# Performance work log

Hardware: AMD Instinct MI355X
Metric: run time of the kernel (lower is better)

## Reference

```python
import jax, jax.numpy as jnp
import numpy as np

B, S, H, NH = 2, 2048, 1024, 16
HD = H // NH  # 64


def setup_inputs() -> dict:
    key = jax.random.key(0)
    ks = jax.random.split(key, 12)
    sc = 0.02
    return {
        "query": jax.random.normal(ks[0], (B, S, H), dtype=jnp.float32),
        "key": jax.random.normal(ks[1], (B, S, H), dtype=jnp.float32),
        "value": jax.random.normal(ks[2], (B, S, H), dtype=jnp.float32),
        "attention_mask": jnp.zeros((B, S, S), dtype=jnp.float32),
        "Wq": jax.random.normal(ks[3], (H, H), dtype=jnp.float32) * sc,
        "bq": jnp.zeros((H,), dtype=jnp.float32),
        "Wk": jax.random.normal(ks[4], (H, H), dtype=jnp.float32) * sc,
        "bk": jnp.zeros((H,), dtype=jnp.float32),
        "Wv": jax.random.normal(ks[5], (H, H), dtype=jnp.float32) * sc,
        "bv": jnp.zeros((H,), dtype=jnp.float32),
        "Wo": jax.random.normal(ks[6], (H, H), dtype=jnp.float32) * sc,
        "bo": jnp.zeros((H,), dtype=jnp.float32),
    }


def reference(query, key, value, attention_mask, Wq, bq, Wk, bk, Wv, bv, Wo, bo):
    b = query.shape[0]
    # linear projections
    q = query @ Wq + bq
    k = key @ Wk + bk
    v = value @ Wv + bv
    # [b, s, h] -> [b, nh, s, hd]
    def split_heads(x):
        return x.reshape(b, -1, NH, HD).transpose(0, 2, 1, 3)
    q, k, v = split_heads(q), split_heads(k), split_heads(v)
    # scaled dot-product attention with materialized score matrix (faithful)
    scores = jnp.einsum("bhqd,bhkd->bhqk", q, k) / jnp.sqrt(jnp.float32(HD))
    scores = scores + attention_mask[:, None, :, :]
    weights = jax.nn.softmax(scores, axis=-1)  # dropout p=0 (eval)
    out = jnp.einsum("bhqk,bhkd->bhqd", weights, v)
    out = out.transpose(0, 2, 1, 3).reshape(b, -1, H)
    return out @ Wo + bo
```

## Files before the change

### kernel.cpp

```cpp
#include <hip/hip_runtime.h>
#include <hip/hip_bf16.h>
#include <math.h>

#define S_  2048
#define H_  1024
#define NH_ 16
#define HD_ 64
#define MM  4096
#define NB_ 2
#define NT_ (S_ / 64)
#define LOG2E 1.44269504088896340736f
#define SMFIX 32.0f

typedef __attribute__((ext_vector_type(8))) short bf16x8;
typedef __attribute__((ext_vector_type(4))) float f32x4;
typedef __attribute__((ext_vector_type(16))) float f32x16;
typedef __attribute__((ext_vector_type(4))) unsigned short us4;
typedef __attribute__((ext_vector_type(8))) unsigned short us8;
typedef __attribute__((ext_vector_type(2))) unsigned uint2v;

__device__ __forceinline__ void gld_lds16(const void* g, void* l) {
    __builtin_amdgcn_global_load_lds(
        (const __attribute__((address_space(1))) unsigned int*)g,
        (__attribute__((address_space(3))) unsigned int*)l, 16, 0, 0);
}

__device__ __forceinline__ unsigned short f2bf(float f) {
    union { float f; unsigned int u; } v; v.f = f;
    unsigned int r = v.u + 0x7FFFu + ((v.u >> 16) & 1u);
    return (unsigned short)(r >> 16);
}

__device__ __forceinline__ unsigned pkbf(float lo, float hi) {
    __hip_bfloat162 h = __float22bfloat162_rn(make_float2(lo, hi));
    unsigned u; __builtin_memcpy(&u, &h, 4); return u;
}

__device__ __forceinline__ float exp2_fast(float x) {
    float r; asm("v_exp_f32 %0, %1" : "=v"(r) : "v"(x)); return r;
}

__global__ __launch_bounds__(256)
void prep_kernel(const float* __restrict__ query, const float* __restrict__ key,
                 const float* __restrict__ value,
                 unsigned short* __restrict__ Xq, unsigned short* __restrict__ Xk,
                 unsigned short* __restrict__ Xv,
                 const float* __restrict__ W0, const float* __restrict__ W1,
                 const float* __restrict__ W2, const float* __restrict__ W3,
                 unsigned short* __restrict__ T0, unsigned short* __restrict__ T1,
                 unsigned short* __restrict__ T2, unsigned short* __restrict__ T3)
{
    __shared__ float t[32][33];
    const int id = blockIdx.x, tid = threadIdx.x;

    if (id < 6144) {
        const int z = id >> 11;
        const float* s = z == 0 ? query : z == 1 ? key : value;
        unsigned short* d = z == 0 ? Xq : z == 1 ? Xk : Xv;
        const int i = (id & 2047) * 256 + tid;
        float4 a = ((const float4*)s)[(size_t)i * 2];
        float4 b = ((const float4*)s)[(size_t)i * 2 + 1];
        union { unsigned u[4]; us8 v; } o;
        o.u[0] = pkbf(a.x, a.y); o.u[1] = pkbf(a.z, a.w);
        o.u[2] = pkbf(b.x, b.y); o.u[3] = pkbf(b.z, b.w);
        ((us8*)d)[i] = o.v;
    } else {
        const int rid = id - 6144;
        const int z = rid >> 10, rem = rid & 1023;
        const int n0 = (rem & 31) * 32, k0 = (rem >> 5) * 32;
        const float* W = z == 0 ? W0 : z == 1 ? W1 : z == 2 ? W2 : W3;
        unsigned short* T = z == 0 ? T0 : z == 1 ? T1 : z == 2 ? T2 : T3;
        const int tx = tid & 31, ty = tid >> 5;
        #pragma unroll
        for (int u = 0; u < 4; u++)
            t[ty + u * 8][tx] = W[(size_t)(k0 + ty + u * 8) * H_ + n0 + tx];
        __syncthreads();
        #pragma unroll
        for (int u = 0; u < 4; u++)
            T[(size_t)(n0 + ty + u * 8) * H_ + k0 + tx] = f2bf(t[tx][ty + u * 8]);
    }
}

__device__ __forceinline__
void gemm_body(unsigned short* As, unsigned short* Bs, int n0, int m0,
               const unsigned short* __restrict__ A, const unsigned short* __restrict__ Bt,
               const float* __restrict__ bias, void* __restrict__ out, float scale, int epi)
{
    const int tid = threadIdx.x;
    const int lane = tid & 63, w = tid >> 6;
    const int lane16 = lane & 15, lg = lane >> 4;
    const int wm = w & 1, wn = w >> 1;

    f32x4 acc[4][4];
    #pragma unroll
    for (int m = 0; m < 4; m++)
        #pragma unroll
        for (int n = 0; n < 4; n++) acc[m][n] = (f32x4){0.f, 0.f, 0.f, 0.f};

    auto stage = [&](int kt) {
        #pragma unroll
        for (int u = 0; u < 4; u++) {
            const int seg = w * 4 + u;
            const int L = seg * 1024 + lane * 16;
            const int row = L >> 7;
            const int blk = (L >> 4) & 7;
            const int goff = kt * 64 + ((blk ^ (row & 7)) << 3);
            gld_lds16(A  + (size_t)(m0 + row) * 1024 + goff, (char*)As + L);
            gld_lds16(Bt + (size_t)(n0 + row) * 1024 + goff, (char*)Bs + L);
        }
    };

    stage(0);
    for (int kt = 0; kt < 16; kt++) {
        __syncthreads();
        #pragma unroll
        for (int ks = 0; ks < 2; ks++) {
            const int kb = ks * 64 + lg * 16;
            bf16x8 a[4], b[4];
            #pragma unroll
            for (int m = 0; m < 4; m++) {
                const int row = wm * 64 + m * 16 + lane16;
                a[m] = *(const bf16x8*)((const char*)As + row * 128 + (kb ^ ((row & 7) << 4)));
            }
            #pragma unroll
            for (int n = 0; n < 4; n++) {
                const int row = wn * 64 + n * 16 + lane16;
                b[n] = *(const bf16x8*)((const char*)Bs + row * 128 + (kb ^ ((row & 7) << 4)));
            }
            #pragma unroll
            for (int m = 0; m < 4; m++)
                #pragma unroll
                for (int n = 0; n < 4; n++)
                    acc[m][n] = __builtin_amdgcn_mfma_f32_16x16x32_bf16(a[m], b[n], acc[m][n], 0, 0, 0);
        }
        __syncthreads();
        if (kt + 1 < 16) stage(kt + 1);
    }

    #pragma unroll
    for (int n = 0; n < 4; n++) {
        const int col = n0 + wn * 64 + n * 16 + lane16;
        const float bs = bias[col];
        #pragma unroll
        for (int m = 0; m < 4; m++) {
            const int rowb = m0 + wm * 64 + m * 16 + lg * 4;
            if (epi == 0) {
                const int nh = col >> 6, hd = col & 63;
                #pragma unroll
                for (int j = 0; j < 4; j++) {
                    const int row = rowb + j;
                    const int bb = row >> 11, s = row & 2047;
                    ((unsigned short*)out)[((((size_t)bb * NH_ + nh) * S_ + s) << 6) + hd] =
                        f2bf((acc[m][n][j] + bs) * scale);
                }
            } else if (epi == 1) {
                const int nh = col >> 6, hd = col & 63;
                const int bb = rowb >> 11, s = rowb & 2047;
                us4 o;
                #pragma unroll
                for (int j = 0; j < 4; j++) o[j] = f2bf(acc[m][n][j] + bs);
                *(us4*)&((unsigned short*)out)[((((size_t)bb * NH_ + nh) * HD_ + hd) << 11) + s] = o;
            } else {
                #pragma unroll
                for (int j = 0; j < 4; j++)
                    ((float*)out)[(size_t)(rowb + j) * H_ + col] = acc[m][n][j] + bs;
            }
        }
    }
}

__global__ __launch_bounds__(256)
void gemm_qkv_mtr(const unsigned short* __restrict__ Xq, const unsigned short* __restrict__ Xk,
                  const unsigned short* __restrict__ Xv,
                  const unsigned short* __restrict__ Wtq, const unsigned short* __restrict__ Wtk,
                  const unsigned short* __restrict__ Wtv,
                  const float* __restrict__ bq, const float* __restrict__ bk,
                  const float* __restrict__ bv,
                  unsigned short* __restrict__ qh, unsigned short* __restrict__ kh,
                  unsigned short* __restrict__ vt, float qscale,
                  const float* __restrict__ M, unsigned short* __restrict__ MT2)
{
    __shared__ __align__(16) unsigned short As[128 * 64];
    __shared__ __align__(16) unsigned short Bs[128 * 64];

    const int id = blockIdx.x, tid = threadIdx.x;

    if (id < 768) {
        const int z = id >> 8, rem = id & 255;
        const int n0 = (rem & 7) * 128, m0 = (rem >> 3) * 128;
        const unsigned short* A  = z == 0 ? Xq : z == 1 ? Xk : Xv;
        const unsigned short* Bt = z == 0 ? Wtq : z == 1 ? Wtk : Wtv;
        const float* bias        = z == 0 ? bq : z == 1 ? bk : bv;
        void* out                = z == 0 ? (void*)qh : z == 1 ? (void*)kh : (void*)vt;
        gemm_body(As, Bs, n0, m0, A, Bt, bias, out, z == 0 ? qscale : 1.0f,
                  z == 2 ? 1 : 0);
    } else {
        float (*t)[33] = (float(*)[33])As;
        const int rid = id - 768;
        const int bz = rid >> 11, rem = rid & 2047;
        const int q0 = (rem & 31) * 64, t2 = rem >> 5;
        const int kv0 = (t2 >> 1) * 64 + (t2 & 1) * 32;
        const float* Mb = M + (size_t)bz * S_ * S_;
        #pragma unroll
        for (int u = 0; u < 2; u++) {
            const int f4 = tid + u * 256;
            const int r = f4 >> 3, c = (f4 & 7) * 4;
            float4 v = *(const float4*)(Mb + (size_t)(q0 + r) * S_ + kv0 + c);
            t[r][c + 0] = v.x; t[r][c + 1] = v.y; t[r][c + 2] = v.z; t[r][c + 3] = v.w;
        }
        __syncthreads();
        const int lg2 = tid >> 7, rem2 = tid & 127;
        const int q = rem2 >> 1, half = rem2 & 1;
        union { unsigned u[4]; us8 v; } o;
        #pragma unroll
        for (int w = 0; w < 4; w++) {
            const int i0 = half * 8 + 2 * w;
            const int kc0 = (i0 & 3) + 8 * (i0 >> 2) + 4 * lg2;
            const int i1 = i0 + 1;
            const int kc1 = (i1 & 3) + 8 * (i1 >> 2) + 4 * lg2;
            o.u[w] = pkbf(fmaf(t[q][kc0], LOG2E, -SMFIX),
                          fmaf(t[q][kc1], LOG2E, -SMFIX));
        }
        const size_t flat = ((((size_t)bz * 64 + t2) * 2 + lg2) * 2048 + (q0 + q)) * 16 + half * 8;
        *(us8*)(MT2 + flat) = o.v;
    }
}

__global__ __launch_bounds__(256)
void gemm_out(const unsigned short* __restrict__ A, const unsigned short* __restrict__ Bt,
              const float* __restrict__ bias, float* __restrict__ out)
{
    __shared__ __align__(16) unsigned short As[128 * 64];
    __shared__ __align__(16) unsigned short Bs[128 * 64];
    gemm_body(As, Bs, blockIdx.x * 128, blockIdx.y * 128, A, Bt, bias, out, 1.0f, 2);
}

__global__ __launch_bounds__(256, 2)
void mfma_attn(const unsigned short* __restrict__ qh, const unsigned short* __restrict__ kh,
               const unsigned short* __restrict__ vt, const unsigned short* __restrict__ maskT,
               unsigned short* __restrict__ ao)
{
    __shared__ __align__(16) unsigned short Ks[2][64 * 64];
    __shared__ __align__(16) unsigned short Vs[2][64 * 64];

    const int tid = threadIdx.x;
    const int lane = tid & 63, wq = tid >> 6;
    const int l31 = lane & 31, lg2 = lane >> 5;
    const int qt = blockIdx.x, h = blockIdx.y, bz = blockIdx.z;
    const int q = qt * 128 + wq * 32 + l31;

    const unsigned short* Kb = kh + ((size_t)(bz * NH_ + h) * S_) * HD_;
    const unsigned short* Vb = vt + ((size_t)(bz * NH_ + h) * HD_) * S_;
    const unsigned short* MT2b = maskT + (size_t)bz * S_ * S_;

    bf16x8 qfrag[4];
    {
        const unsigned short* Qrow = qh + (((size_t)(bz * NH_ + h) * S_) + q) * HD_;
        #pragma unroll
        for (int s = 0; s < 4; s++)
            qfrag[s] = *(const bf16x8*)(Qrow + s * 16 + lg2 * 8);
    }

    auto stageKV = [&](int t) {
        const int buf = t & 1;
        #pragma unroll
        for (int u = 0; u < 2; u++) {
            const int L = u * 4096 + tid * 16;
            const int row = L >> 7, blk = (L >> 4) & 7;
            const int off = (blk ^ (row & 7)) << 3;
            gld_lds16(Kb + (size_t)(t * 64 + row) * HD_ + off, (char*)&Ks[buf][0] + L);
            gld_lds16(Vb + (size_t)row * S_ + t * 64 + off,    (char*)&Vs[buf][0] + L);
        }
    };
    stageKV(0);

    us8 mpA[2][2], mpB[2][2];
    auto loadMT = [&](int t, us8 (&mp)[2][2]) {
        #pragma unroll
        for (int bb = 0; bb < 2; bb++) {
            const unsigned short* src = MT2b +
                ((((size_t)(t * 2 + bb)) * 2 + lg2) * 2048 + q) * 16;
            mp[bb][0] = *(const us8*)(src);
            mp[bb][1] = *(const us8*)(src + 8);
        }
    };
    loadMT(0, mpA);

    __syncthreads();

    f32x16 oacc[2];
    #pragma unroll
    for (int db = 0; db < 2; db++)
        #pragma unroll
        for (int i = 0; i < 16; i++) oacc[db][i] = 0.f;
    float l_run = 0.f;

    auto tile = [&](int t, us8 (&Mc)[2][2], us8 (&Mn)[2][2]) {
        if (t) __syncthreads();
        const int buf = t & 1;

        if (t + 1 < NT_) { stageKV(t + 1); loadMT(t + 1, Mn); }

        f32x16 sc[2];
        __builtin_amdgcn_s_setprio(1);
        #pragma unroll
        for (int bb = 0; bb < 2; bb++) {
            f32x16 a;
            #pragma unroll
            for (int i = 0; i < 16; i++) a[i] = 0.f;
            #pragma unroll
            for (int s = 0; s < 4; s++) {
                const int row = bb * 32 + l31;
                bf16x8 kf = *(const bf16x8*)((const char*)&Ks[buf][0] + row * 128 +
                                             ((s * 32 + lg2 * 16) ^ ((row & 7) << 4)));
                a = __builtin_amdgcn_mfma_f32_32x32x16_bf16(kf, qfrag[s], a, 0, 0, 0);
            }
            sc[bb] = a;
        }
        __builtin_amdgcn_s_setprio(0);

        #pragma unroll
        for (int bb = 0; bb < 2; bb++) {
            union { us8 v; unsigned u[4]; } h0, h1;
            h0.v = Mc[bb][0]; h1.v = Mc[bb][1];
            #pragma unroll
            for (int i = 0; i < 16; i++) {
                const unsigned wrd = (i < 8) ? h0.u[i >> 1] : h1.u[(i - 8) >> 1];
                const float mf = __uint_as_float((i & 1) ? (wrd & 0xFFFF0000u)
                                                         : (wrd << 16));
                sc[bb][i] = exp2_fast(sc[bb][i] + mf);
            }
        }
        float s8[8];
        #pragma unroll
        for (int i = 0; i < 8; i++)
            s8[i] = (sc[0][i] + sc[0][i + 8]) + (sc[1][i] + sc[1][i + 8]);
        l_run += ((s8[0] + s8[1]) + (s8[2] + s8[3])) + ((s8[4] + s8[5]) + (s8[6] + s8[7]));

        bf16x8 pfrag[4];
        #pragma unroll
        for (int bb = 0; bb < 2; bb++)
            #pragma unroll
            for (int g = 0; g < 2; g++) {
                const int o = g * 8;
                unsigned X0 = pkbf(sc[bb][o + 0], sc[bb][o + 1]);
                unsigned X1 = pkbf(sc[bb][o + 2], sc[bb][o + 3]);
                unsigned Y0 = pkbf(sc[bb][o + 4], sc[bb][o + 5]);
                unsigned Y1 = pkbf(sc[bb][o + 6], sc[bb][o + 7]);
                uint2v r0 = __builtin_amdgcn_permlane32_swap(X0, Y0, false, false);
                uint2v r1 = __builtin_amdgcn_permlane32_swap(X1, Y1, false, false);
                union { unsigned u[4]; bf16x8 v; } P;
                P.u[0] = r0.x; P.u[1] = r1.x; P.u[2] = r0.y; P.u[3] = r1.y;
                pfrag[bb * 2 + g] = P.v;
            }

        __builtin_amdgcn_s_setprio(1);
        #pragma unroll
        for (int s = 0; s < 4; s++)
            #pragma unroll
            for (int db = 0; db < 2; db++) {
                const int row = db * 32 + l31;
                bf16x8 vf = *(const bf16x8*)((const char*)&Vs[buf][0] + row * 128 +
                                             ((s * 32 + lg2 * 16) ^ ((row & 7) << 4)));
                oacc[db] = __builtin_amdgcn_mfma_f32_32x32x16_bf16(vf, pfrag[s], oacc[db], 0, 0, 0);
            }
        __builtin_amdgcn_s_setprio(0);
    };

    for (int tt = 0; tt < NT_; tt += 2) {
        tile(tt,     mpA, mpB);
        tile(tt + 1, mpB, mpA);
    }

    l_run += __shfl_xor(l_run, 32, 64);
    const float inv = 1.0f / l_run;
    unsigned short* aoq = ao + ((size_t)(bz * S_ + q)) * H_ + h * HD_;
    #pragma unroll
    for (int db = 0; db < 2; db++)
        #pragma unroll
        for (int m = 0; m < 4; m++) {
            us4 o = { f2bf(oacc[db][m * 4 + 0] * inv), f2bf(oacc[db][m * 4 + 1] * inv),
                      f2bf(oacc[db][m * 4 + 2] * inv), f2bf(oacc[db][m * 4 + 3] * inv) };
            *(us4*)&aoq[db * 32 + m * 8 + lg2 * 4] = o;
        }
}

extern "C" void kernel_launch(void* const* d_in, const int* in_sizes, int n_in,
                              void* d_out, int out_size, void* d_ws, size_t ws_size,
                              hipStream_t stream)
{
    (void)in_sizes; (void)n_in; (void)out_size; (void)ws_size;

    const float* query = (const float*)d_in[0];
    const float* key   = (const float*)d_in[1];
    const float* value = (const float*)d_in[2];
    const float* mask  = (const float*)d_in[3];
    const float* Wq    = (const float*)d_in[4];
    const float* bq    = (const float*)d_in[5];
    const float* Wk    = (const float*)d_in[6];
    const float* bk    = (const float*)d_in[7];
    const float* Wv    = (const float*)d_in[8];
    const float* bv    = (const float*)d_in[9];
    const float* Wo    = (const float*)d_in[10];
    const float* bo    = (const float*)d_in[11];

    unsigned short* ws = (unsigned short*)d_ws;
    const size_t MH = (size_t)MM * H_;
    const size_t WW = (size_t)H_ * H_;
    unsigned short* Xq  = ws;
    unsigned short* Xk  = Xq + MH;
    unsigned short* Xv  = Xk + MH;
    unsigned short* maskT = Xv + MH;
    unsigned short* Wtq = maskT + 2 * MH;
    unsigned short* Wtk = Wtq + WW;
    unsigned short* Wtv = Wtk + WW;
    unsigned short* Wto = Wtv + WW;
    unsigned short* qh  = Wto + WW;
    unsigned short* kh  = qh + MH;
    unsigned short* vt  = kh + MH;
    unsigned short* ao  = vt + MH;

    prep_kernel<<<dim3(10240), 256, 0, stream>>>(
        query, key, value, Xq, Xk, Xv,
        Wq, Wk, Wv, Wo, Wtq, Wtk, Wtv, Wto);

    gemm_qkv_mtr<<<dim3(768 + 4096), 256, 0, stream>>>(
        Xq, Xk, Xv, Wtq, Wtk, Wtv, bq, bk, bv,
        qh, kh, vt, 0.125f * LOG2E, mask, maskT);

    mfma_attn<<<dim3(S_ / 128, NH_, NB_), 256, 0, stream>>>(qh, kh, vt, maskT, ao);

    gemm_out<<<dim3(8, 32), 256, 0, stream>>>(ao, Wto, bo, (float*)d_out);
}
```

Before: 140.2 us.

## Swizzle block IDs across XCDs and move Wo transpose into QKV kernel

Remaps linear block IDs in the QKV GEMM, attention and output GEMM kernels so that consecutive blocks dispatched round-robin to the 8 XCDs work on neighbouring tiles or heads. This should improve L2 reuse of shared K/V and weight tiles. The Wo transpose/convert is also moved out of the prep kernel into the QKV GEMM launch, which shortens the critical prep kernel and lets that work overlap with the GEMM tail. The cost is extra index arithmetic and some risk of load imbalance.

```diff
diff --git a/kernel.cpp b/kernel.cpp
--- a/kernel.cpp
+++ b/kernel.cpp
@@ -46,9 +46,9 @@
                  unsigned short* __restrict__ Xq, unsigned short* __restrict__ Xk,
                  unsigned short* __restrict__ Xv,
                  const float* __restrict__ W0, const float* __restrict__ W1,
-                 const float* __restrict__ W2, const float* __restrict__ W3,
+                 const float* __restrict__ W2,
                  unsigned short* __restrict__ T0, unsigned short* __restrict__ T1,
-                 unsigned short* __restrict__ T2, unsigned short* __restrict__ T3)
+                 unsigned short* __restrict__ T2)
 {
     __shared__ float t[32][33];
     const int id = blockIdx.x, tid = threadIdx.x;
@@ -68,8 +68,8 @@
         const int rid = id - 6144;
         const int z = rid >> 10, rem = rid & 1023;
         const int n0 = (rem & 31) * 32, k0 = (rem >> 5) * 32;
-        const float* W = z == 0 ? W0 : z == 1 ? W1 : z == 2 ? W2 : W3;
-        unsigned short* T = z == 0 ? T0 : z == 1 ? T1 : z == 2 ? T2 : T3;
+        const float* W = z == 0 ? W0 : z == 1 ? W1 : W2;
+        unsigned short* T = z == 0 ? T0 : z == 1 ? T1 : T2;
         const int tx = tid & 31, ty = tid >> 5;
         #pragma unroll
         for (int u = 0; u < 4; u++)
@@ -178,6 +178,7 @@
                   const float* __restrict__ bv,
                   unsigned short* __restrict__ qh, unsigned short* __restrict__ kh,
                   unsigned short* __restrict__ vt, float qscale,
+                  const float* __restrict__ Wo, unsigned short* __restrict__ Wto,
                   const float* __restrict__ M, unsigned short* __restrict__ MT2)
 {
     __shared__ __align__(16) unsigned short As[128 * 64];
@@ -186,7 +187,8 @@
     const int id = blockIdx.x, tid = threadIdx.x;
 
     if (id < 768) {
-        const int z = id >> 8, rem = id & 255;
+        const int wg = (id & 7) * 96 + (id >> 3);
+        const int z = wg >> 8, rem = wg & 255;
         const int n0 = (rem & 7) * 128, m0 = (rem >> 3) * 128;
         const unsigned short* A  = z == 0 ? Xq : z == 1 ? Xk : Xv;
         const unsigned short* Bt = z == 0 ? Wtq : z == 1 ? Wtk : Wtv;
@@ -194,9 +196,21 @@
         void* out                = z == 0 ? (void*)qh : z == 1 ? (void*)kh : (void*)vt;
         gemm_body(As, Bs, n0, m0, A, Bt, bias, out, z == 0 ? qscale : 1.0f,
                   z == 2 ? 1 : 0);
+    } else if (id < 1792) {
+        float (*t)[33] = (float(*)[33])As;
+        const int rid = id - 768;
+        const int n0 = (rid & 31) * 32, k0 = (rid >> 5) * 32;
+        const int tx = tid & 31, ty = tid >> 5;
+        #pragma unroll
+        for (int u = 0; u < 4; u++)
+            t[ty + u * 8][tx] = Wo[(size_t)(k0 + ty + u * 8) * H_ + n0 + tx];
+        __syncthreads();
+        #pragma unroll
+        for (int u = 0; u < 4; u++)
+            Wto[(size_t)(n0 + ty + u * 8) * H_ + k0 + tx] = f2bf(t[tx][ty + u * 8]);
     } else {
         float (*t)[33] = (float(*)[33])As;
-        const int rid = id - 768;
+        const int rid = id - 1792;
         const int bz = rid >> 11, rem = rid & 2047;
         const int q0 = (rem & 31) * 64, t2 = rem >> 5;
         const int kv0 = (t2 >> 1) * 64 + (t2 & 1) * 32;
@@ -232,7 +246,9 @@
 {
     __shared__ __align__(16) unsigned short As[128 * 64];
     __shared__ __align__(16) unsigned short Bs[128 * 64];
-    gemm_body(As, Bs, blockIdx.x * 128, blockIdx.y * 128, A, Bt, bias, out, 1.0f, 2);
+    const int id = blockIdx.x;
+    const int wg = (id & 7) * 32 + (id >> 3);
+    gemm_body(As, Bs, (wg & 7) * 128, (wg >> 3) * 128, A, Bt, bias, out, 1.0f, 2);
 }
 
 __global__ __launch_bounds__(256, 2)
@@ -246,7 +262,9 @@
     const int tid = threadIdx.x;
     const int lane = tid & 63, wq = tid >> 6;
     const int l31 = lane & 31, lg2 = lane >> 5;
-    const int qt = blockIdx.x, h = blockIdx.y, bz = blockIdx.z;
+
+    const int wg = ((blockIdx.x & 7) << 6) + (blockIdx.x >> 3);
+    const int qt = wg & 15, h = (wg >> 4) & 15, bz = wg >> 8;
     const int q = qt * 128 + wq * 32 + l31;
 
     const unsigned short* Kb = kh + ((size_t)(bz * NH_ + h) * S_) * HD_;
@@ -420,15 +438,15 @@
     unsigned short* vt  = kh + MH;
     unsigned short* ao  = vt + MH;
 
-    prep_kernel<<<dim3(10240), 256, 0, stream>>>(
+    prep_kernel<<<dim3(9216), 256, 0, stream>>>(
         query, key, value, Xq, Xk, Xv,
-        Wq, Wk, Wv, Wo, Wtq, Wtk, Wtv, Wto);
-
-    gemm_qkv_mtr<<<dim3(768 + 4096), 256, 0, stream>>>(
+        Wq, Wk, Wv, Wtq, Wtk, Wtv);
+
+    gemm_qkv_mtr<<<dim3(768 + 1024 + 4096), 256, 0, stream>>>(
         Xq, Xk, Xv, Wtq, Wtk, Wtv, bq, bk, bv,
-        qh, kh, vt, 0.125f * LOG2E, mask, maskT);
-
-    mfma_attn<<<dim3(S_ / 128, NH_, NB_), 256, 0, stream>>>(qh, kh, vt, maskT, ao);
-
-    gemm_out<<<dim3(8, 32), 256, 0, stream>>>(ao, Wto, bo, (float*)d_out);
-}
+        qh, kh, vt, 0.125f * LOG2E, Wo, Wto, mask, maskT);
+
+    mfma_attn<<<dim3(512), 256, 0, stream>>>(qh, kh, vt, maskT, ao);
+
+    gemm_out<<<dim3(256), 256, 0, stream>>>(ao, Wto, bo, (float*)d_out);
+}
```

Result: faster. 132.7 us (-5.3%).
